# Optimization experiments

Hardware: AMD Instinct MI355X
Metric: run time of the kernel (lower is better)

Reference implementation:

```python
import jax, jax.numpy as jnp
import numpy as np

OBS, HID, LAT = 1024, 2048, 256
VOCAB, HQ = 8192, 4
COMMIT = 0.5
N = 16384
LN_EPS = 1e-5


def setup_inputs() -> dict:
    key = jax.random.key(0)
    ks = jax.random.split(key, 7)

    def lin_w(k, fan_in, shape):
        # torch nn.Linear default init: U(-1/sqrt(fan_in), 1/sqrt(fan_in))
        bound = 1.0 / np.sqrt(fan_in)
        return jax.random.uniform(k, shape, jnp.float32, -bound, bound)

    return {
        "x": jax.random.normal(ks[0], (N, OBS), jnp.float32),
        # embeddings initialized uniform(-0.5, 0.5) as in the module
        "codebooks": jax.random.uniform(ks[1], (HQ, VOCAB, LAT), jnp.float32, -0.5, 0.5),
        "enc_w1": lin_w(ks[2], OBS, (OBS, HID)),
        "enc_b1": jnp.zeros((HID,), jnp.float32),
        "ln_g": jnp.ones((HID,), jnp.float32),
        "ln_b": jnp.zeros((HID,), jnp.float32),
        "enc_w2": lin_w(ks[3], HID, (HID, LAT)),
        "enc_b2": jnp.zeros((LAT,), jnp.float32),
        "dec_w1": lin_w(ks[4], LAT, (LAT, HID)),
        "dec_b1": jnp.zeros((HID,), jnp.float32),
        "dec_w2": lin_w(ks[5], HID, (HID, OBS)),
        "dec_b2": jnp.zeros((OBS,), jnp.float32),
    }


def reference(x, codebooks, enc_w1, enc_b1, ln_g, ln_b, enc_w2, enc_b2,
              dec_w1, dec_b1, dec_w2, dec_b2):
    sg = jax.lax.stop_gradient
    # encoder: Linear -> LayerNorm -> ReLU -> Linear
    h = x @ enc_w1 + enc_b1                      # [N, HID]
    mu = h.mean(-1, keepdims=True)
    var = ((h - mu) ** 2).mean(-1, keepdims=True)  # biased var, matches torch LN
    h = (h - mu) * jax.lax.rsqrt(var + LN_EPS) * ln_g + ln_b
    h = jax.nn.relu(h)
    latent = h @ enc_w2 + enc_b2                 # [N, LAT]

    total = jnp.float32(0.0)
    resid = latent
    code_sum = jnp.zeros_like(latent)
    for l in range(HQ):
        E = codebooks[l]                         # [VOCAB, LAT]
        # squared euclidean distances (argmin identical to cdist argmin)
        d2 = ((resid * resid).sum(-1, keepdims=True)
              - 2.0 * (resid @ E.T)
              + (E * E).sum(-1))                 # [N, VOCAB]
        idx = jnp.argmin(d2, axis=-1)            # [N]
        q = E[idx]                               # [N, LAT] gather
        codebook_loss = jnp.mean((q - sg(resid)) ** 2)
        commit_loss = jnp.mean((sg(q) - resid) ** 2)
        total = total + codebook_loss + COMMIT * commit_loss
        code_sum = code_sum + q
        resid = resid - q

    # straight-through estimator
    quant = latent + sg(code_sum - latent)
    # decoder: Linear -> ReLU -> Linear
    dh = jax.nn.relu(quant @ dec_w1 + dec_b1)
    recon = dh @ dec_w2 + dec_b2                 # [N, OBS]
    total = total + 0.5 * jnp.mean((recon - x) ** 2)
    return total
```

## Files before the change

kernel.cpp:

```cpp
#include <hip/hip_runtime.h>

#define N_ROWS 16384
#define OBS    1024
#define HID    2048
#define LAT    256
#define VOCAB  8192
#define HQ     4
#define LN_EPS 1e-5f

typedef unsigned short u16;
typedef unsigned long long u64;
typedef __bf16 bf16x8 __attribute__((ext_vector_type(8)));
typedef float  f32x4  __attribute__((ext_vector_type(4)));

static __device__ __forceinline__ unsigned int float_to_ordered(float f) {
    unsigned int u = __float_as_uint(f);
    return (u & 0x80000000u) ? ~u : (u | 0x80000000u);
}
static __device__ __forceinline__ u16 f2bf(float f) {
    unsigned int u = __float_as_uint(f);
    unsigned int r = u + 0x7FFFu + ((u >> 16) & 1u);
    return (u16)(r >> 16);
}
static __device__ __forceinline__ float bf2f(u16 u) {
    return __uint_as_float((unsigned int)u << 16);
}

#define GL2LDS(gp, lp) __builtin_amdgcn_global_load_lds( \
    (const __attribute__((address_space(1))) void*)(gp), \
    (__attribute__((address_space(3))) void*)(lp), 16, 0, 0)

template<int EPI>
__global__ __launch_bounds__(256, 4) void mfma_gemm_k(
    const u16* __restrict__ Abf, const u16* __restrict__ Bbf,
    const float* __restrict__ bias,
    u16* __restrict__ Cbf,
    const float* __restrict__ X, double* __restrict__ lacc,
    int K, int Nd)
{
    __shared__ u16 As[128 * 64];
    __shared__ u16 Bs[128 * 64];

    const int tid  = threadIdx.x;
    const int wv   = tid >> 6, lane = tid & 63;
    const int wm   = wv & 1,   wn   = wv >> 1;
    const int m_   = lane & 15, g   = lane >> 4;
    const int m0   = blockIdx.x * 128;
    const int n0   = blockIdx.y * 128;

    f32x4 acc[4][4];
#pragma unroll
    for (int i = 0; i < 4; ++i)
#pragma unroll
        for (int j = 0; j < 4; ++j)
            acc[i][j] = f32x4{0.f, 0.f, 0.f, 0.f};

    const u16* Ablk = Abf + (size_t)m0 * K;
    const u16* Bblk = Bbf + (size_t)n0 * K;

    for (int k0 = 0; k0 < K; k0 += 64) {
#pragma unroll
        for (int c = 0; c < 4; ++c) {
            const int ci = (wv * 4 + c) * 64 + lane;
            const int r  = ci >> 3;
            const int cc = ci & 7;
            const int kc = (cc ^ (r & 7)) << 3;
            GL2LDS(Ablk + (size_t)r * K + k0 + kc, As + (wv * 4 + c) * 512);
            GL2LDS(Bblk + (size_t)r * K + k0 + kc, Bs + (wv * 4 + c) * 512);
        }
        __syncthreads();
#pragma unroll
        for (int ks = 0; ks < 2; ++ks) {
            const int ccw = ks * 4 + g;
            const int sw  = (ccw ^ (m_ & 7)) << 3;
            bf16x8 af[4], bfr[4];
#pragma unroll
            for (int t = 0; t < 4; ++t) {
                af[t]  = *(const bf16x8*)&As[(wm * 64 + t * 16 + m_) * 64 + sw];
                bfr[t] = *(const bf16x8*)&Bs[(wn * 64 + t * 16 + m_) * 64 + sw];
            }
#pragma unroll
            for (int mi = 0; mi < 4; ++mi)
#pragma unroll
                for (int ni = 0; ni < 4; ++ni)
                    acc[mi][ni] = __builtin_amdgcn_mfma_f32_16x16x32_bf16(
                        af[mi], bfr[ni], acc[mi][ni], 0, 0, 0);
        }
        __syncthreads();
    }

    float bs[4];
#pragma unroll
    for (int ni = 0; ni < 4; ++ni) bs[ni] = bias[n0 + wn * 64 + ni * 16 + m_];

    if constexpr (EPI == 3) {
        float lsum = 0.f;
#pragma unroll
        for (int mi = 0; mi < 4; ++mi)
#pragma unroll
            for (int j = 0; j < 4; ++j) {
                const int row = m0 + wm * 64 + mi * 16 + g * 4 + j;
#pragma unroll
                for (int ni = 0; ni < 4; ++ni) {
                    const int col = n0 + wn * 64 + ni * 16 + m_;
                    float r = acc[mi][ni][j] + bs[ni] - X[(size_t)row * Nd + col];
                    lsum = fmaf(r, r, lsum);
                }
            }
#pragma unroll
        for (int off = 32; off >= 1; off >>= 1) lsum += __shfl_xor(lsum, off);
        __shared__ float red[4];
        if (lane == 0) red[wv] = lsum;
        __syncthreads();
        if (tid == 0)
            atomicAdd(lacc, (double)(red[0] + red[1] + red[2] + red[3]));
    } else {
#pragma unroll
        for (int mi = 0; mi < 4; ++mi)
#pragma unroll
            for (int j = 0; j < 4; ++j) {
                const int row = m0 + wm * 64 + mi * 16 + g * 4 + j;
#pragma unroll
                for (int ni = 0; ni < 4; ++ni) {
                    const int col = n0 + wn * 64 + ni * 16 + m_;
                    float v = acc[mi][ni][j] + bs[ni];
                    if constexpr (EPI == 1) v = fmaxf(v, 0.f);
                    Cbf[(size_t)row * Nd + col] = f2bf(v);
                }
            }
    }
}

__global__ __launch_bounds__(256, 4) void gemm2_k(
    const u16* __restrict__ Abf, const u16* __restrict__ Bbf,
    const float* __restrict__ bias,
    float* __restrict__ lat, float* __restrict__ resid, u16* __restrict__ rbf)
{
    __shared__ u16 As[64 * 64];
    __shared__ u16 Bs[64 * 64];

    const int tid = threadIdx.x;
    const int wv  = tid >> 6, lane = tid & 63;
    const int wm  = wv & 1,   wn   = wv >> 1;
    const int m_  = lane & 15, g   = lane >> 4;
    const int m0  = blockIdx.x * 64;
    const int n0  = blockIdx.y * 64;

    f32x4 acc[2][2];
#pragma unroll
    for (int i = 0; i < 2; ++i)
#pragma unroll
        for (int j = 0; j < 2; ++j)
            acc[i][j] = f32x4{0.f, 0.f, 0.f, 0.f};

    const u16* Ablk = Abf + (size_t)m0 * HID;
    const u16* Bblk = Bbf + (size_t)n0 * HID;

    for (int k0 = 0; k0 < HID; k0 += 64) {
#pragma unroll
        for (int c = 0; c < 2; ++c) {
            const int ci = (wv * 2 + c) * 64 + lane;
            const int r  = ci >> 3;
            const int cc = ci & 7;
            const int kc = (cc ^ (r & 7)) << 3;
            GL2LDS(Ablk + (size_t)r * HID + k0 + kc, As + (wv * 2 + c) * 512);
            GL2LDS(Bblk + (size_t)r * HID + k0 + kc, Bs + (wv * 2 + c) * 512);
        }
        __syncthreads();
#pragma unroll
        for (int ks = 0; ks < 2; ++ks) {
            const int ccw = ks * 4 + g;
            const int sw  = (ccw ^ (m_ & 7)) << 3;
            bf16x8 af[2], bfr[2];
#pragma unroll
            for (int t = 0; t < 2; ++t) {
                af[t]  = *(const bf16x8*)&As[(wm * 32 + t * 16 + m_) * 64 + sw];
                bfr[t] = *(const bf16x8*)&Bs[(wn * 32 + t * 16 + m_) * 64 + sw];
            }
#pragma unroll
            for (int mi = 0; mi < 2; ++mi)
#pragma unroll
                for (int ni = 0; ni < 2; ++ni)
                    acc[mi][ni] = __builtin_amdgcn_mfma_f32_16x16x32_bf16(
                        af[mi], bfr[ni], acc[mi][ni], 0, 0, 0);
        }
        __syncthreads();
    }

#pragma unroll
    for (int mi = 0; mi < 2; ++mi)
#pragma unroll
        for (int j = 0; j < 4; ++j) {
            const int row = m0 + wm * 32 + mi * 16 + g * 4 + j;
#pragma unroll
            for (int ni = 0; ni < 2; ++ni) {
                const int col = n0 + wn * 32 + ni * 16 + m_;
                float v = acc[mi][ni][j] + bias[col];
                lat  [(size_t)row * LAT + col] = v;
                resid[(size_t)row * LAT + col] = v;
                rbf  [(size_t)row * LAT + col] = f2bf(v);
            }
        }
}

__global__ __launch_bounds__(256) void tpose4_k(
    const float* __restrict__ W0, u16* __restrict__ T0,
    const float* __restrict__ W1, u16* __restrict__ T1,
    const float* __restrict__ W2, u16* __restrict__ T2,
    const float* __restrict__ W3, u16* __restrict__ T3)
{
    __shared__ u16 t[32][33];
    const int bid = blockIdx.x;
    const float* W; u16* T; int K, N, r;
    if (bid < 2048)      { W = W0; T = T0; K = OBS; N = HID; r = bid; }
    else if (bid < 2560) { W = W1; T = T1; K = HID; N = LAT; r = bid - 2048; }
    else if (bid < 3072) { W = W2; T = T2; K = LAT; N = HID; r = bid - 2560; }
    else                 { W = W3; T = T3; K = HID; N = OBS; r = bid - 3072; }
    const int nb = N >> 5;
    const int n0 = (r % nb) * 32, k0 = (r / nb) * 32;
    const int lx = threadIdx.x & 31, ly = threadIdx.x >> 5;
#pragma unroll
    for (int i = 0; i < 4; ++i)
        t[ly + 8 * i][lx] = f2bf(W[(size_t)(k0 + ly + 8 * i) * N + n0 + lx]);
    __syncthreads();
#pragma unroll
    for (int i = 0; i < 4; ++i)
        T[(size_t)(n0 + ly + 8 * i) * K + k0 + lx] = t[lx][ly + 8 * i];
}

__device__ __forceinline__ float block_reduce_bcast(float v, float* scratch) {
#pragma unroll
    for (int off = 32; off >= 1; off >>= 1) v += __shfl_xor(v, off);
    const int tid = threadIdx.x;
    __syncthreads();
    if ((tid & 63) == 0) scratch[tid >> 6] = v;
    __syncthreads();
    return scratch[0] + scratch[1] + scratch[2] + scratch[3];
}

__global__ __launch_bounds__(256) void ln_relu_bf_k(
    u16* __restrict__ h, const float* __restrict__ g, const float* __restrict__ b)
{
    __shared__ float scratch[4];
    const int tid = threadIdx.x;
    u16* hp = h + (size_t)blockIdx.x * HID + tid * 8;

    ushort4 r0 = *(const ushort4*)hp;
    ushort4 r1 = *(const ushort4*)(hp + 4);
    float v[8] = {bf2f(r0.x), bf2f(r0.y), bf2f(r0.z), bf2f(r0.w),
                  bf2f(r1.x), bf2f(r1.y), bf2f(r1.z), bf2f(r1.w)};

    float s = 0.f;
#pragma unroll
    for (int e = 0; e < 8; ++e) s += v[e];
    const float mu = block_reduce_bcast(s, scratch) * (1.f / HID);

    float vs = 0.f;
#pragma unroll
    for (int e = 0; e < 8; ++e) { float d = v[e] - mu; vs = fmaf(d, d, vs); }
    const float var = block_reduce_bcast(vs, scratch) * (1.f / HID);
    const float rs = rsqrtf(var + LN_EPS);

    ushort4 o0, o1;
#pragma unroll
    for (int e = 0; e < 8; ++e) {
        const int col = tid * 8 + e;
        float w = (v[e] - mu) * rs * g[col] + b[col];
        w = fmaxf(w, 0.f);
        u16 bb = f2bf(w);
        if (e < 4) ((u16*)&o0)[e] = bb; else ((u16*)&o1)[e - 4] = bb;
    }
    *(ushort4*)hp = o0;
    *(ushort4*)(hp + 4) = o1;
}

__global__ __launch_bounds__(256) void enorm_k(
    const float* __restrict__ cb, float* __restrict__ enorm,
    u16* __restrict__ cbb, u64* __restrict__ keys, double* __restrict__ accs)
{
    if (blockIdx.x < 64) keys[blockIdx.x * 256 + threadIdx.x] = ~0ull;
    if (blockIdx.x == 64 && threadIdx.x < 2) accs[threadIdx.x] = 0.0;
    const int row  = blockIdx.x * 4 + (threadIdx.x >> 6);
    const int lane = threadIdx.x & 63;
    const size_t off = (size_t)row * LAT + lane * 4;
    float4 v = *(const float4*)(cb + off);
    ushort4 o;
    o.x = f2bf(-2.f * v.x); o.y = f2bf(-2.f * v.y);
    o.z = f2bf(-2.f * v.z); o.w = f2bf(-2.f * v.w);
    *(ushort4*)(cbb + off) = o;
    float s = v.x * v.x + v.y * v.y + v.z * v.z + v.w * v.w;
#pragma unroll
    for (int off2 = 32; off2 >= 1; off2 >>= 1) s += __shfl_xor(s, off2);
    if (lane == 0) enorm[row] = s;
}

__global__ __launch_bounds__(256) void f2bf_k(
    const float* __restrict__ in, u16* __restrict__ out)
{
    size_t i = ((size_t)blockIdx.x * 256 + threadIdx.x) * 4;
    float4 v = *(const float4*)(in + i);
    ushort4 o;
    o.x = f2bf(v.x); o.y = f2bf(v.y); o.z = f2bf(v.z); o.w = f2bf(v.w);
    *(ushort4*)(out + i) = o;
}

__global__ __launch_bounds__(256, 4) void dist_mfma_k(
    const u16* __restrict__ Abf, const u16* __restrict__ Bneg2,
    const float* __restrict__ enorm, u64* __restrict__ keys)
{
    __shared__ u16 As[128 * 64];
    __shared__ u16 Bs[128 * 64];
    __shared__ u64 shk[128][2];

    const int tid  = threadIdx.x;
    const int wv   = tid >> 6, lane = tid & 63;
    const int wm   = wv & 1,   wn   = wv >> 1;
    const int m_   = lane & 15, g   = lane >> 4;
    const int m0   = blockIdx.x * 128;
    const int n0   = blockIdx.y * 128;

    f32x4 acc[4][4];
#pragma unroll
    for (int ni = 0; ni < 4; ++ni) {
        const float en = enorm[n0 + wn * 64 + ni * 16 + m_];
#pragma unroll
        for (int mi = 0; mi < 4; ++mi)
            acc[mi][ni] = f32x4{en, en, en, en};
    }

    const u16* Ablk = Abf   + (size_t)m0 * LAT;
    const u16* Bblk = Bneg2 + (size_t)n0 * LAT;

    for (int k0 = 0; k0 < LAT; k0 += 64) {
#pragma unroll
        for (int c = 0; c < 4; ++c) {
            const int ci = (wv * 4 + c) * 64 + lane;
            const int r  = ci >> 3;
            const int cc = ci & 7;
            const int kc = (cc ^ (r & 7)) << 3;
            GL2LDS(Ablk + (size_t)r * LAT + k0 + kc, As + (wv * 4 + c) * 512);
            GL2LDS(Bblk + (size_t)r * LAT + k0 + kc, Bs + (wv * 4 + c) * 512);
        }
        __syncthreads();
#pragma unroll
        for (int ks = 0; ks < 2; ++ks) {
            const int ccw = ks * 4 + g;
            const int sw  = (ccw ^ (m_ & 7)) << 3;
            bf16x8 af[4], bfr[4];
#pragma unroll
            for (int t = 0; t < 4; ++t) {
                af[t]  = *(const bf16x8*)&As[(wm * 64 + t * 16 + m_) * 64 + sw];
                bfr[t] = *(const bf16x8*)&Bs[(wn * 64 + t * 16 + m_) * 64 + sw];
            }
#pragma unroll
            for (int mi = 0; mi < 4; ++mi)
#pragma unroll
                for (int ni = 0; ni < 4; ++ni)
                    acc[mi][ni] = __builtin_amdgcn_mfma_f32_16x16x32_bf16(
                        af[mi], bfr[ni], acc[mi][ni], 0, 0, 0);
        }
        __syncthreads();
    }

#pragma unroll
    for (int mi = 0; mi < 4; ++mi)
#pragma unroll
        for (int j = 0; j < 4; ++j) {
            float bs_ = acc[mi][0][j];
            int   bi_ = n0 + wn * 64 + m_;
#pragma unroll
            for (int ni = 1; ni < 4; ++ni) {
                const float s = acc[mi][ni][j];
                const int   v = n0 + wn * 64 + ni * 16 + m_;
                if (s < bs_) { bs_ = s; bi_ = v; }
            }
            u64 best = ((u64)float_to_ordered(bs_) << 32) | (unsigned)bi_;
#pragma unroll
            for (int mask = 1; mask <= 8; mask <<= 1) {
                u64 o = __shfl_xor(best, mask);
                best = o < best ? o : best;
            }
            if (m_ == 0) shk[wm * 64 + mi * 16 + g * 4 + j][wn] = best;
        }
    __syncthreads();
    if (tid < 128) {
        u64 a = shk[tid][0], b = shk[tid][1];
        atomicMin(&keys[m0 + tid], a < b ? a : b);
    }
}

template<bool LAST>
__global__ __launch_bounds__(256) void vq_update_k(
    float* __restrict__ resid, u16* __restrict__ aux,
    const float* __restrict__ latent,
    const float* __restrict__ E,
    u64* __restrict__ keys, double* __restrict__ acc)
{
    __shared__ float red[4];
    const int tid = threadIdx.x;
    const int base = blockIdx.x * 16;
    float lsum = 0.f;
    for (int r = 0; r < 16; ++r) {
        const int row = base + r;
        const int idx = (int)(keys[row] & 0xFFFFFFFFull);
        const float q = E[(size_t)idx * LAT + tid];
        float v = resid[(size_t)row * LAT + tid] - q;
        if constexpr (LAST) {
            aux[(size_t)row * LAT + tid] =
                f2bf(latent[(size_t)row * LAT + tid] - v);
        } else {
            resid[(size_t)row * LAT + tid] = v;
            aux[(size_t)row * LAT + tid] = f2bf(v);
        }
        lsum = fmaf(v, v, lsum);
    }
    if (!LAST && tid < 16) keys[base + tid] = ~0ull;
#pragma unroll
    for (int off = 32; off >= 1; off >>= 1) lsum += __shfl_xor(lsum, off);
    if ((tid & 63) == 0) red[tid >> 6] = lsum;
    __syncthreads();
    if (tid == 0) atomicAdd(acc, (double)(red[0] + red[1] + red[2] + red[3]));
}

__global__ void finalize_k(const double* __restrict__ acc, float* __restrict__ out) {
    double total = 1.5 * acc[0] / (double)((size_t)N_ROWS * LAT)
                 + 0.5 * acc[1] / (double)((size_t)N_ROWS * OBS);
    out[0] = (float)total;
}

extern "C" void kernel_launch(void* const* d_in, const int* in_sizes, int n_in,
                              void* d_out, int out_size, void* d_ws, size_t ws_size,
                              hipStream_t stream)
{
    const float* x      = (const float*)d_in[0];
    const float* cb     = (const float*)d_in[1];
    const float* enc_w1 = (const float*)d_in[2];
    const float* enc_b1 = (const float*)d_in[3];
    const float* ln_g   = (const float*)d_in[4];
    const float* ln_b   = (const float*)d_in[5];
    const float* enc_w2 = (const float*)d_in[6];
    const float* enc_b2 = (const float*)d_in[7];
    const float* dec_w1 = (const float*)d_in[8];
    const float* dec_b1 = (const float*)d_in[9];
    const float* dec_w2 = (const float*)d_in[10];
    const float* dec_b2 = (const float*)d_in[11];

    char* ws = (char*)d_ws;
    const size_t MB = 1ull << 20;
    u16* hbuf = (u16*)ws;
    u16* cbb  = (u16*)(ws + 64 * MB);
    u16* rbf  = (u16*)(ws + 80 * MB);
    u16* qbf  = (u16*)(ws + 88 * MB);
    u16* xbf  = (u16*)(ws + 96 * MB);
    float* latent = (float*)(ws + 96 * MB);
    float* resid  = (float*)(ws + 112 * MB);
    u16* w1T  = (u16*)(ws + 128 * MB);
    u16* w2T  = (u16*)(ws + 132 * MB);
    u16* wd1T = (u16*)(ws + 133 * MB);
    u16* wd2T = (u16*)(ws + 134 * MB);
    float* enorm = (float*)(ws + 138 * MB);
    u64*   keys  = (u64*)(ws + 138 * MB + 131072);
    double* accs = (double*)(ws + 138 * MB + 262144);

    enorm_k<<<HQ * VOCAB / 4, 256, 0, stream>>>(cb, enorm, cbb, keys, accs);

    tpose4_k<<<5120, 256, 0, stream>>>(enc_w1, w1T, enc_w2, w2T,
                                       dec_w1, wd1T, dec_w2, wd2T);
    f2bf_k<<<(int)((size_t)N_ROWS * OBS / 1024), 256, 0, stream>>>(x, xbf);

    mfma_gemm_k<0><<<dim3(N_ROWS / 128, HID / 128), 256, 0, stream>>>(
        xbf, w1T, enc_b1, hbuf, nullptr, nullptr, OBS, HID);
    ln_relu_bf_k<<<N_ROWS, 256, 0, stream>>>(hbuf, ln_g, ln_b);
    gemm2_k<<<dim3(N_ROWS / 64, LAT / 64), 256, 0, stream>>>(
        hbuf, w2T, enc_b2, latent, resid, rbf);

    for (int l = 0; l < HQ; ++l) {
        dist_mfma_k<<<dim3(N_ROWS / 128, VOCAB / 128), 256, 0, stream>>>(
            rbf, cbb + (size_t)l * VOCAB * LAT, enorm + (size_t)l * VOCAB, keys);
        if (l < HQ - 1)
            vq_update_k<false><<<N_ROWS / 16, 256, 0, stream>>>(
                resid, rbf, nullptr, cb + (size_t)l * VOCAB * LAT, keys, accs);
        else
            vq_update_k<true><<<N_ROWS / 16, 256, 0, stream>>>(
                resid, qbf, latent, cb + (size_t)l * VOCAB * LAT, keys, accs);
    }

    mfma_gemm_k<1><<<dim3(N_ROWS / 128, HID / 128), 256, 0, stream>>>(
        qbf, wd1T, dec_b1, hbuf, nullptr, nullptr, LAT, HID);
    mfma_gemm_k<3><<<dim3(N_ROWS / 128, OBS / 128), 256, 0, stream>>>(
        hbuf, wd2T, dec_b2, nullptr, x, accs + 1, HID, OBS);

    finalize_k<<<1, 1, 0, stream>>>(accs, (float*)d_out);
}
```

Baseline: 891.4 us.

## Keep residual tile in registers and stream codebook tiles with double-buffered LDS

The distance kernel now loads its 128-row residual slice once into registers (full K=256) and loops over 16 codebook tiles of 64 entries, double-buffering those tiles in LDS via async global-to-LDS copies. A running per-row argmin is kept in registers across tiles, so each block writes far fewer atomicMin updates and no longer reloads A for every codebook tile. The grid shrinks by a factor of 8 in the vocab dimension and launch bounds drop to 2 blocks per SM, which trades occupancy for more register and LDS reuse.

```diff
diff --git a/kernel.cpp b/kernel.cpp
--- a/kernel.cpp
+++ b/kernel.cpp
@@ -304,12 +304,13 @@
     *(ushort4*)(out + i) = o;
 }
 
-__global__ __launch_bounds__(256, 4) void dist_mfma_k(
+#define DNT 16
+
+__global__ __launch_bounds__(256, 2) void dist_mfma_k(
     const u16* __restrict__ Abf, const u16* __restrict__ Bneg2,
     const float* __restrict__ enorm, u64* __restrict__ keys)
 {
-    __shared__ u16 As[128 * 64];
-    __shared__ u16 Bs[128 * 64];
+    __shared__ u16 Bs[2][64 * 256];
     __shared__ u64 shk[128][2];
 
     const int tid  = threadIdx.x;
@@ -317,70 +318,105 @@
     const int wm   = wv & 1,   wn   = wv >> 1;
     const int m_   = lane & 15, g   = lane >> 4;
     const int m0   = blockIdx.x * 128;
-    const int n0   = blockIdx.y * 128;
-
-    f32x4 acc[4][4];
-#pragma unroll
-    for (int ni = 0; ni < 4; ++ni) {
-        const float en = enorm[n0 + wn * 64 + ni * 16 + m_];
+    const int c0   = blockIdx.y * (64 * DNT);
+
+    bf16x8 af[4][8];
+    {
+        const u16* Ablk = Abf + (size_t)m0 * LAT;
+#pragma unroll
+        for (int mi = 0; mi < 4; ++mi) {
+            const u16* rp = Ablk + (size_t)(wm * 64 + mi * 16 + m_) * LAT + g * 8;
+#pragma unroll
+            for (int kk = 0; kk < 8; ++kk)
+                af[mi][kk] = *(const bf16x8*)(rp + kk * 32);
+        }
+    }
+
+    const u16* Bbase = Bneg2 + (size_t)c0 * LAT;
+
+    u64 best[4][4];
+#pragma unroll
+    for (int mi = 0; mi < 4; ++mi)
+#pragma unroll
+        for (int j4 = 0; j4 < 4; ++j4) best[mi][j4] = ~0ull;
+
+    auto stageB = [&](int j, int buf) {
+#pragma unroll
+        for (int t = 0; t < 4; ++t)
+#pragma unroll
+            for (int c = 0; c < 2; ++c) {
+                const int idx = (wv * 2 + c) * 64 + lane;
+                const int r   = idx >> 3;
+                const int cc  = idx & 7;
+                const int kc  = (cc ^ (r & 7)) << 3;
+                GL2LDS(Bbase + (size_t)(j * 64 + r) * LAT + t * 64 + kc,
+                       &Bs[buf][t * 4096 + (wv * 2 + c) * 512]);
+            }
+    };
+
+    stageB(0, 0);
+    __syncthreads();
+
+    for (int j = 0; j < DNT; ++j) {
+        const int cur = j & 1;
+        if (j + 1 < DNT) stageB(j + 1, cur ^ 1);
+
+        const int bc  = c0 + j * 64 + wn * 32 + m_;
+        const float en0 = enorm[bc];
+        const float en1 = enorm[bc + 16];
+        f32x4 acc[4][2];
+#pragma unroll
+        for (int mi = 0; mi < 4; ++mi) {
+            acc[mi][0] = f32x4{en0, en0, en0, en0};
+            acc[mi][1] = f32x4{en1, en1, en1, en1};
+        }
+
+        const u16* bsc = &Bs[cur][0];
+#pragma unroll
+        for (int kc_ = 0; kc_ < 4; ++kc_)
+#pragma unroll
+            for (int ks = 0; ks < 2; ++ks) {
+                const int ccw = ks * 4 + g;
+                const int sw  = (ccw ^ (m_ & 7)) << 3;
+                bf16x8 b0 = *(const bf16x8*)
+                    &bsc[kc_ * 4096 + (wn * 32 + m_) * 64 + sw];
+                bf16x8 b1 = *(const bf16x8*)
+                    &bsc[kc_ * 4096 + (wn * 32 + 16 + m_) * 64 + sw];
+                const int kk = kc_ * 2 + ks;
+#pragma unroll
+                for (int mi = 0; mi < 4; ++mi) {
+                    acc[mi][0] = __builtin_amdgcn_mfma_f32_16x16x32_bf16(
+                        af[mi][kk], b0, acc[mi][0], 0, 0, 0);
+                    acc[mi][1] = __builtin_amdgcn_mfma_f32_16x16x32_bf16(
+                        af[mi][kk], b1, acc[mi][1], 0, 0, 0);
+                }
+            }
+
 #pragma unroll
         for (int mi = 0; mi < 4; ++mi)
-            acc[mi][ni] = f32x4{en, en, en, en};
-    }
-
-    const u16* Ablk = Abf   + (size_t)m0 * LAT;
-    const u16* Bblk = Bneg2 + (size_t)n0 * LAT;
-
-    for (int k0 = 0; k0 < LAT; k0 += 64) {
-#pragma unroll
-        for (int c = 0; c < 4; ++c) {
-            const int ci = (wv * 4 + c) * 64 + lane;
-            const int r  = ci >> 3;
-            const int cc = ci & 7;
-            const int kc = (cc ^ (r & 7)) << 3;
-            GL2LDS(Ablk + (size_t)r * LAT + k0 + kc, As + (wv * 4 + c) * 512);
-            GL2LDS(Bblk + (size_t)r * LAT + k0 + kc, Bs + (wv * 4 + c) * 512);
-        }
+#pragma unroll
+            for (int j4 = 0; j4 < 4; ++j4) {
+                const float s0 = acc[mi][0][j4];
+                const float s1 = acc[mi][1][j4];
+                u64 p0 = ((u64)float_to_ordered(s0) << 32) | (unsigned)bc;
+                u64 p1 = ((u64)float_to_ordered(s1) << 32) | (unsigned)(bc + 16);
+                u64 p  = p0 < p1 ? p0 : p1;
+                if (p < best[mi][j4]) best[mi][j4] = p;
+            }
         __syncthreads();
-#pragma unroll
-        for (int ks = 0; ks < 2; ++ks) {
-            const int ccw = ks * 4 + g;
-            const int sw  = (ccw ^ (m_ & 7)) << 3;
-            bf16x8 af[4], bfr[4];
-#pragma unroll
-            for (int t = 0; t < 4; ++t) {
-                af[t]  = *(const bf16x8*)&As[(wm * 64 + t * 16 + m_) * 64 + sw];
-                bfr[t] = *(const bf16x8*)&Bs[(wn * 64 + t * 16 + m_) * 64 + sw];
-            }
-#pragma unroll
-            for (int mi = 0; mi < 4; ++mi)
-#pragma unroll
-                for (int ni = 0; ni < 4; ++ni)
-                    acc[mi][ni] = __builtin_amdgcn_mfma_f32_16x16x32_bf16(
-                        af[mi], bfr[ni], acc[mi][ni], 0, 0, 0);
-        }
-        __syncthreads();
     }
 
 #pragma unroll
     for (int mi = 0; mi < 4; ++mi)
 #pragma unroll
-        for (int j = 0; j < 4; ++j) {
-            float bs_ = acc[mi][0][j];
-            int   bi_ = n0 + wn * 64 + m_;
-#pragma unroll
-            for (int ni = 1; ni < 4; ++ni) {
-                const float s = acc[mi][ni][j];
-                const int   v = n0 + wn * 64 + ni * 16 + m_;
-                if (s < bs_) { bs_ = s; bi_ = v; }
-            }
-            u64 best = ((u64)float_to_ordered(bs_) << 32) | (unsigned)bi_;
+        for (int j4 = 0; j4 < 4; ++j4) {
+            u64 b = best[mi][j4];
 #pragma unroll
             for (int mask = 1; mask <= 8; mask <<= 1) {
-                u64 o = __shfl_xor(best, mask);
-                best = o < best ? o : best;
-            }
-            if (m_ == 0) shk[wm * 64 + mi * 16 + g * 4 + j][wn] = best;
+                u64 o = __shfl_xor(b, mask);
+                b = o < b ? o : b;
+            }
+            if (m_ == 0) shk[wm * 64 + mi * 16 + g * 4 + j4][wn] = b;
         }
     __syncthreads();
     if (tid < 128) {
@@ -475,7 +511,7 @@
         hbuf, w2T, enc_b2, latent, resid, rbf);
 
     for (int l = 0; l < HQ; ++l) {
-        dist_mfma_k<<<dim3(N_ROWS / 128, VOCAB / 128), 256, 0, stream>>>(
+        dist_mfma_k<<<dim3(N_ROWS / 128, VOCAB / (64 * DNT)), 256, 0, stream>>>(
             rbf, cbb + (size_t)l * VOCAB * LAT, enorm + (size_t)l * VOCAB, keys);
         if (l < HQ - 1)
             vq_update_k<false><<<N_ROWS / 16, 256, 0, stream>>>(
```

After: 801.6 us. 10.1% less time.
